# Kernel optimization log

Hardware: AMD Instinct MI355X
Metric: run time of the kernel (lower is better)

Reference implementation:

```python
import jax, jax.numpy as jnp
import numpy as np

INNER = 64  # hardcoded inner_dim in the torch module


def _knn_idx(pos, k):
    # dgcnn-style knn: topk of negative squared distance (includes self)
    d2 = jnp.sum(pos * pos, axis=-1)                      # (b, n)
    sim = 2.0 * jnp.einsum('bic,bjc->bij', pos, pos) - d2[:, :, None] - d2[:, None, :]
    return jax.lax.top_k(sim, k)[1]                       # (b, n, k)


def setup_inputs() -> dict:
    key = jax.random.key(0)
    ks = jax.random.split(key, 16)
    emb_dim = 256
    b, n, k = 8, 2048, 16
    s = 0.05
    inp = {
        'x': jax.random.normal(ks[0], (b, n, emb_dim), dtype=jnp.float32),
        'pos': jax.random.normal(ks[1], (b, n, 3), dtype=jnp.float32),
        'w_qkv': jax.random.normal(ks[2], (emb_dim, 3 * INNER), dtype=jnp.float32) * s,
        'w_pos1': jax.random.normal(ks[3], (3, 64), dtype=jnp.float32) * s,
        'b_pos1': jnp.zeros((64,), dtype=jnp.float32),
        'w_pos2': jax.random.normal(ks[4], (64, INNER), dtype=jnp.float32) * s,
        'b_pos2': jnp.zeros((INNER,), dtype=jnp.float32),
        'w_att1': jax.random.normal(ks[5], (INNER, 4 * INNER), dtype=jnp.float32) * s,
        'b_att1': jnp.zeros((4 * INNER,), dtype=jnp.float32),
        'w_att2': jax.random.normal(ks[6], (4 * INNER, INNER), dtype=jnp.float32) * s,
        'b_att2': jnp.zeros((INNER,), dtype=jnp.float32),
        'w_out': jax.random.normal(ks[7], (INNER, emb_dim), dtype=jnp.float32) * s,
        'b_out': jnp.zeros((emb_dim,), dtype=jnp.float32),
        'k': k,
    }
    return inp


def reference(x, pos, w_qkv, w_pos1, b_pos1, w_pos2, b_pos2,
              w_att1, b_att1, w_att2, b_att2, w_out, b_out, k):
    b, n, _ = x.shape
    qkv = x @ w_qkv                                        # (b, n, 3*INNER)
    q, kk, v = jnp.split(qkv, 3, axis=-1)                  # each (b, n, INNER)

    idx = _knn_idx(pos, k) + (jnp.arange(b) * n)[:, None, None]  # flat offsets
    idxf = idx.reshape(-1)

    def gather(t, d):
        return jnp.take(t.reshape(b * n, d), idxf, axis=0).reshape(b, n, k, d)

    pos_nn = gather(pos, 3)                                # (b, n, k, 3)
    rel_pos = pos_nn - pos[:, :, None, :]
    rpe = jax.nn.relu(rel_pos @ w_pos1 + b_pos1) @ w_pos2 + b_pos2  # (b, n, k, INNER)

    q_nn = gather(q, INNER)
    k_nn = gather(kk, INNER)
    v_nn = gather(v, INNER) + rpe

    h = q_nn - k_nn + rpe
    sim = jax.nn.relu(h @ w_att1 + b_att1) @ w_att2 + b_att2       # (b, n, k, INNER)

    # NOTE: faithful to torch source — softmax over the CHANNEL dim (-1),
    # then L2-normalize over the neighbor dim (-2).
    attn = jax.nn.softmax(sim, axis=-1)
    norm = jnp.sqrt(jnp.sum(attn * attn, axis=-2, keepdims=True))
    attn = attn / jnp.maximum(norm, 1e-12)

    agg = jnp.sum(attn * v_nn, axis=2)                     # (b, n, INNER)
    return agg @ w_out + b_out                             # (b, n, emb_dim)
```

## Files before the change

### kernel.cpp

```cpp
#include <hip/hip_runtime.h>
#include <stdint.h>

typedef __attribute__((ext_vector_type(8))) short bf8v;
typedef __attribute__((ext_vector_type(4))) float f4v;
typedef __attribute__((ext_vector_type(4))) unsigned int u4v;
typedef __attribute__((ext_vector_type(2))) unsigned int u2v;

#define MFMA16(a,b,c) __builtin_amdgcn_mfma_f32_16x16x32_bf16((a),(b),(c),0,0,0)

__device__ __forceinline__ unsigned short f2bf(float f) {
    unsigned u = __float_as_uint(f);
    return (unsigned short)((u + 0x7FFFu + ((u >> 16) & 1u)) >> 16);
}
#define SW(row,k,L) ((row)*(L) + ((k) ^ (((row)&7)<<3)))

#define WS_QMK   0u
#define WS_V     4194304u
#define WS_AGG   8388608u
#define WS_IDX   12582912u
#define WS_W1T   13631488u
#define WS_W2T   13664256u
#define WS_WPT   13697024u
#define WS_WQK   13705216u
#define WS_WOUT  13770752u

__global__ __launch_bounds__(256) void k_prep(
    const float* __restrict__ w_qkv, const float* __restrict__ w_pos2,
    const float* __restrict__ w_att1, const float* __restrict__ w_att2,
    const float* __restrict__ w_out, char* __restrict__ ws)
{
    int t = blockIdx.x * 256 + threadIdx.x;
    unsigned short* w1i = (unsigned short*)(ws + WS_W1T);
    unsigned short* w2i = (unsigned short*)(ws + WS_W2T);
    unsigned short* wpi = (unsigned short*)(ws + WS_WPT);
    unsigned short* wqi = (unsigned short*)(ws + WS_WQK);
    unsigned short* woi = (unsigned short*)(ws + WS_WOUT);
    if (t < 16384) {
        int hid = t >> 6, k = t & 63;
        w1i[hid*64 + (k ^ ((hid&7)<<3))] = f2bf(w_att1[k*256 + hid]);
    } else if (t < 32768) {
        int i = t - 16384; int ch = i >> 8, k = i & 255;
        w2i[ch*256 + (k ^ ((ch&7)<<3))] = f2bf(w_att2[k*64 + ch]);
    } else if (t < 36864) {
        int i = t - 32768; int ch = i >> 6, k = i & 63;
        wpi[ch*64 + (k ^ ((ch&7)<<3))] = f2bf(w_pos2[k*64 + ch]);
    } else if (t < 69632) {
        int i = t - 36864; int col = i >> 8, k = i & 255;
        float val = (col < 64) ? (w_qkv[k*192 + col] - w_qkv[k*192 + 64 + col])
                               : w_qkv[k*192 + 128 + (col - 64)];
        wqi[col*256 + (k ^ ((col&7)<<3))] = f2bf(val);
    } else if (t < 86016) {
        int i = t - 69632; int col = i >> 6, k = i & 63;
        woi[col*64 + (k ^ ((col&7)<<3))] = f2bf(w_out[k*256 + col]);
    }
}

__global__ __launch_bounds__(256) void k_knn(const float* __restrict__ pos,
                                             int* __restrict__ idxo) {
    const int wid = threadIdx.x >> 6, lane = threadIdx.x & 63;
    const int pid = blockIdx.x * 4 + wid;
    const int b = pid >> 11, i = pid & 2047;
    const float* pb = pos + (size_t)b * 2048 * 3;
    float xi = pb[i*3], yi = pb[i*3+1], zi = pb[i*3+2];
    float d2i = xi*xi; d2i = fmaf(yi, yi, d2i); d2i = fmaf(zi, zi, d2i);
    unsigned long long key[32];
#pragma unroll
    for (int m = 0; m < 32; ++m) {
        int j = m * 64 + lane;
        float xj = pb[j*3], yj = pb[j*3+1], zj = pb[j*3+2];
        float d2j = xj*xj; d2j = fmaf(yj, yj, d2j); d2j = fmaf(zj, zj, d2j);
        float dot = xi*xj; dot = fmaf(yi, yj, dot); dot = fmaf(zi, zj, dot);
        float sim = 2.0f*dot - d2i - d2j;
        unsigned u = __float_as_uint(sim);
        unsigned fk = (u & 0x80000000u) ? ~u : (u | 0x80000000u);
        key[m] = ((unsigned long long)fk << 32) | (unsigned)(0xFFFFFFFFu - (unsigned)j);
    }
    unsigned long long lmax = key[0];
#pragma unroll
    for (int m = 1; m < 32; ++m) lmax = (key[m] > lmax) ? key[m] : lmax;
    int my = 0;
    for (int it = 0; it < 16; ++it) {
        unsigned long long wmax = lmax;
#pragma unroll
        for (int st = 32; st >= 1; st >>= 1) {
            unsigned long long o = __shfl_xor(wmax, st);
            wmax = (o > wmax) ? o : wmax;
        }
        int jw = (int)(0xFFFFFFFFu - (unsigned)(wmax & 0xFFFFFFFFull));
        if (lane == it) my = jw;
        if (lmax == wmax) {
#pragma unroll
            for (int m = 0; m < 32; ++m) if (key[m] == wmax) key[m] = 0ull;
            lmax = key[0];
#pragma unroll
            for (int m = 1; m < 32; ++m) lmax = (key[m] > lmax) ? key[m] : lmax;
        }
    }
    if (lane < 16) idxo[pid * 16 + lane] = b * 2048 + my;
}

__global__ __launch_bounds__(256, 1) void k_qkv(const float* __restrict__ x,
        const char* __restrict__ wimg, float* __restrict__ qmk, float* __restrict__ v) {
    extern __shared__ char smem[];
    unsigned short* WQ = (unsigned short*)smem;
    unsigned short* XT = (unsigned short*)(smem + 65536);
    const int tid = threadIdx.x, wid = tid >> 6, lane = tid & 63;
    const int q4 = lane >> 4, l15 = lane & 15;
#pragma unroll
    for (int itn = 0; itn < 16; ++itn) {
        int off = itn * 4096 + tid * 16;
        *(u4v*)(smem + off) = *(const u4v*)(wimg + off);
    }
    __syncthreads();
    {
        int r = tid >> 2, k64 = (tid & 3) * 64;
        const float* xr = x + ((size_t)blockIdx.x * 64 + r) * 256 + k64;
#pragma unroll
        for (int c = 0; c < 8; ++c) {
            f4v a = *(const f4v*)(xr + c*8);
            f4v bq = *(const f4v*)(xr + c*8 + 4);
            bf8v s;
            s[0]=(short)f2bf(a[0]); s[1]=(short)f2bf(a[1]); s[2]=(short)f2bf(a[2]); s[3]=(short)f2bf(a[3]);
            s[4]=(short)f2bf(bq[0]); s[5]=(short)f2bf(bq[1]); s[6]=(short)f2bf(bq[2]); s[7]=(short)f2bf(bq[3]);
            *(bf8v*)&XT[SW(r, k64 + c*8, 256)] = s;
        }
    }
    f4v z = {0.f,0.f,0.f,0.f};
    f4v acc[8];
#pragma unroll
    for (int n = 0; n < 8; ++n) acc[n] = z;
    const int arow = wid*16 + l15;
#pragma unroll
    for (int ks = 0; ks < 8; ++ks) {
        int k0 = ks*32 + q4*8;
        bf8v a = *(const bf8v*)&XT[SW(arow, k0, 256)];
#pragma unroll
        for (int nt = 0; nt < 8; ++nt) {
            bf8v bq = *(const bf8v*)&WQ[SW(nt*16 + l15, k0, 256)];
            acc[nt] = MFMA16(a, bq, acc[nt]);
        }
    }
    size_t rbase = (size_t)blockIdx.x * 64 + wid*16 + q4*4;
#pragma unroll
    for (int nt = 0; nt < 8; ++nt) {
        int col = nt*16 + l15;
#pragma unroll
        for (int j = 0; j < 4; ++j) {
            if (nt < 4) qmk[(rbase + j)*64 + col] = acc[nt][j];
            else        v[(rbase + j)*64 + (col - 64)] = acc[nt][j];
        }
    }
}

__global__ __launch_bounds__(512, 2) void k_att(
    const float* __restrict__ qmk, const float* __restrict__ v,
    const float* __restrict__ pos, const int* __restrict__ idx,
    const float* __restrict__ w_pos1, const float* __restrict__ b_pos1,
    const float* __restrict__ b_pos2, const float* __restrict__ b_att1,
    const float* __restrict__ b_att2, const char* __restrict__ wblob,
    float* __restrict__ agg)
{
    extern __shared__ char smem[];
    unsigned short* W1T = (unsigned short*)smem;
    unsigned short* W2T = (unsigned short*)(smem + 32768);
    unsigned short* WPT = (unsigned short*)(smem + 65536);
    const int tid = threadIdx.x, wid = tid >> 6, lane = tid & 63;
    const int q4 = lane >> 4, l15 = lane & 15;
    const int r4 = lane >> 2, c16 = (lane & 3) * 16;
    char* wb = smem + 73728 + wid * 10240;
    unsigned short* P  = (unsigned short*)wb;
    unsigned short* PH = (unsigned short*)wb;
    unsigned short* H  = (unsigned short*)(wb + 8192);

#pragma unroll
    for (int it = 0; it < 9; ++it) {
        int off = it * 8192 + tid * 16;
        *(u4v*)(smem + off) = *(const u4v*)(wblob + off);
    }
    __syncthreads();

#pragma unroll 1
    for (int g = 0; g < 8; ++g) {
        const int p = (blockIdx.x * 8 + wid) * 8 + g;
        const int rowbase = p * 16;

        const int flat_l = idx[rowbase + l15];
        f4v qk[4], vv[4];
#pragma unroll
        for (int mt = 0; mt < 4; ++mt)
            qk[mt] = *(const f4v*)(qmk + (size_t)flat_l * 64 + mt*16 + q4*4);
#pragma unroll
        for (int mt = 0; mt < 4; ++mt)
            vv[mt] = *(const f4v*)(v + (size_t)flat_l * 64 + mt*16 + q4*4);

        {
            int flat_r = idx[rowbase + r4];
            float cx = pos[p*3], cy = pos[p*3+1], cz = pos[p*3+2];
            float r0 = pos[flat_r*3] - cx, r1 = pos[flat_r*3+1] - cy, r2v = pos[flat_r*3+2] - cz;
            bf8v lo, hi;
#pragma unroll
            for (int u = 0; u < 4; ++u) {
                f4v w0 = *(const f4v*)(w_pos1 + c16 + u*4);
                f4v w1 = *(const f4v*)(w_pos1 + 64 + c16 + u*4);
                f4v w2 = *(const f4v*)(w_pos1 + 128 + c16 + u*4);
                f4v bb = *(const f4v*)(b_pos1 + c16 + u*4);
#pragma unroll
                for (int j = 0; j < 4; ++j) {
                    float t = fmaf(r2v, w2[j], fmaf(r1, w1[j], fmaf(r0, w0[j], bb[j])));
                    t = fmaxf(t, 0.f);
                    if (u < 2) lo[u*4+j] = (short)f2bf(t);
                    else       hi[(u-2)*4+j] = (short)f2bf(t);
                }
            }
            *(bf8v*)&PH[SW(r4, c16, 64)] = lo;
            *(bf8v*)&PH[SW(r4, c16+8, 64)] = hi;
        }

        f4v rp[4];
#pragma unroll
        for (int mt = 0; mt < 4; ++mt) rp[mt] = *(const f4v*)(b_pos2 + mt*16 + q4*4);
#pragma unroll
        for (int ks = 0; ks < 2; ++ks) {
            int k0 = ks*32 + q4*8;
            bf8v bfr = *(const bf8v*)&PH[SW(l15, k0, 64)];
#pragma unroll
            for (int mt = 0; mt < 4; ++mt)
                rp[mt] = MFMA16(*(const bf8v*)&WPT[SW(mt*16+l15, k0, 64)], bfr, rp[mt]);
        }

        f4v vn[4];
#pragma unroll
        for (int mt = 0; mt < 4; ++mt) {
            float h0 = rp[mt][0] + qk[mt][0], h1 = rp[mt][1] + qk[mt][1];
            float h2 = rp[mt][2] + qk[mt][2], h3 = rp[mt][3] + qk[mt][3];
            u2v pp;
            pp[0] = (unsigned)f2bf(h0) | ((unsigned)f2bf(h1) << 16);
            pp[1] = (unsigned)f2bf(h2) | ((unsigned)f2bf(h3) << 16);
            *(u2v*)&H[SW(l15, mt*16 + q4*4, 64)] = pp;
            vn[mt] = rp[mt] + vv[mt];
        }

        f4v c1[16];
#pragma unroll
        for (int mt = 0; mt < 16; ++mt) c1[mt] = *(const f4v*)(b_att1 + mt*16 + q4*4);
#pragma unroll
        for (int ks = 0; ks < 2; ++ks) {
            int k0 = ks*32 + q4*8;
            bf8v bfr = *(const bf8v*)&H[SW(l15, k0, 64)];
#pragma unroll
            for (int mt = 0; mt < 16; ++mt)
                c1[mt] = MFMA16(*(const bf8v*)&W1T[SW(mt*16+l15, k0, 64)], bfr, c1[mt]);
        }

#pragma unroll
        for (int mt = 0; mt < 16; ++mt) {
            float t0 = fmaxf(c1[mt][0], 0.f), t1 = fmaxf(c1[mt][1], 0.f);
            float t2 = fmaxf(c1[mt][2], 0.f), t3 = fmaxf(c1[mt][3], 0.f);
            u2v pp;
            pp[0] = (unsigned)f2bf(t0) | ((unsigned)f2bf(t1) << 16);
            pp[1] = (unsigned)f2bf(t2) | ((unsigned)f2bf(t3) << 16);
            *(u2v*)&P[SW(l15, mt*16 + q4*4, 256)] = pp;
        }

        f4v ss[4];
#pragma unroll
        for (int mt = 0; mt < 4; ++mt) ss[mt] = *(const f4v*)(b_att2 + mt*16 + q4*4);
#pragma unroll
        for (int ks = 0; ks < 8; ++ks) {
            int k0 = ks*32 + q4*8;
            bf8v bfr = *(const bf8v*)&P[SW(l15, k0, 256)];
#pragma unroll
            for (int mt = 0; mt < 4; ++mt)
                ss[mt] = MFMA16(*(const bf8v*)&W2T[SW(mt*16+l15, k0, 256)], bfr, ss[mt]);
        }

        float e[16]; float mx = -3.4e38f;
#pragma unroll
        for (int i = 0; i < 16; ++i) { e[i] = ss[i>>2][i&3]; mx = fmaxf(mx, e[i]); }
        mx = fmaxf(mx, __shfl_xor(mx, 16));
        mx = fmaxf(mx, __shfl_xor(mx, 32));
        float sum = 0.f;
#pragma unroll
        for (int i = 0; i < 16; ++i) { e[i] = __expf(e[i] - mx); sum += e[i]; }
        sum += __shfl_xor(sum, 16);
        sum += __shfl_xor(sum, 32);
        float inv = 1.0f / sum;
        float nn[16], av[16];
#pragma unroll
        for (int i = 0; i < 16; ++i) {
            e[i] *= inv;
            nn[i] = e[i] * e[i];
            av[i] = e[i] * vn[i>>2][i&3];
        }
#pragma unroll
        for (int st = 1; st <= 8; st <<= 1) {
#pragma unroll
            for (int i = 0; i < 16; ++i) {
                nn[i] += __shfl_xor(nn[i], st);
                av[i] += __shfl_xor(av[i], st);
            }
        }
        if (l15 == 0) {
#pragma unroll
            for (int mt = 0; mt < 4; ++mt) {
                f4v o;
#pragma unroll
                for (int j = 0; j < 4; ++j)
                    o[j] = av[mt*4+j] / fmaxf(sqrtf(nn[mt*4+j]), 1e-12f);
                *(f4v*)(agg + (size_t)p*64 + mt*16 + q4*4) = o;
            }
        }
    }
}

__global__ __launch_bounds__(256, 1) void k_out(const float* __restrict__ agg,
        const char* __restrict__ wimg, const float* __restrict__ b_out,
        float* __restrict__ outp) {
    extern __shared__ char smem[];
    unsigned short* WO = (unsigned short*)smem;
    unsigned short* AT = (unsigned short*)(smem + 32768);
    const int tid = threadIdx.x, wid = tid >> 6, lane = tid & 63;
    const int q4 = lane >> 4, l15 = lane & 15;
#pragma unroll
    for (int itn = 0; itn < 8; ++itn) {
        int off = itn * 4096 + tid * 16;
        *(u4v*)(smem + off) = *(const u4v*)(wimg + off);
    }
    __syncthreads();
    {
        int r = tid >> 2, k16 = (tid & 3) * 16;
        const float* ar = agg + ((size_t)blockIdx.x * 64 + r) * 64 + k16;
        bf8v lo, hi;
#pragma unroll
        for (int i = 0; i < 16; ++i) {
            float t = ar[i];
            if (i < 8) lo[i] = (short)f2bf(t); else hi[i-8] = (short)f2bf(t);
        }
        *(bf8v*)&AT[SW(r, k16, 64)] = lo;
        *(bf8v*)&AT[SW(r, k16+8, 64)] = hi;
    }
    f4v z = {0.f,0.f,0.f,0.f};
    f4v acc[16];
#pragma unroll
    for (int nt = 0; nt < 16; ++nt) acc[nt] = z;
#pragma unroll
    for (int ks = 0; ks < 2; ++ks) {
        int k0 = ks*32 + q4*8;
        bf8v a = *(const bf8v*)&AT[SW(wid*16 + l15, k0, 64)];
#pragma unroll
        for (int nt = 0; nt < 16; ++nt) {
            bf8v bq = *(const bf8v*)&WO[SW(nt*16 + l15, k0, 64)];
            acc[nt] = MFMA16(a, bq, acc[nt]);
        }
    }
    size_t rbase = (size_t)blockIdx.x * 64 + wid*16 + q4*4;
#pragma unroll
    for (int nt = 0; nt < 16; ++nt) {
        int col = nt*16 + l15;
        float bo = b_out[col];
#pragma unroll
        for (int j = 0; j < 4; ++j)
            outp[(rbase + j)*256 + col] = acc[nt][j] + bo;
    }
}

extern "C" void kernel_launch(void* const* d_in, const int* in_sizes, int n_in,
                              void* d_out, int out_size, void* d_ws, size_t ws_size,
                              hipStream_t stream) {
    (void)in_sizes; (void)n_in; (void)out_size; (void)ws_size;
    const float* x      = (const float*)d_in[0];
    const float* pos    = (const float*)d_in[1];
    const float* w_qkv  = (const float*)d_in[2];
    const float* w_pos1 = (const float*)d_in[3];
    const float* b_pos1 = (const float*)d_in[4];
    const float* w_pos2 = (const float*)d_in[5];
    const float* b_pos2 = (const float*)d_in[6];
    const float* w_att1 = (const float*)d_in[7];
    const float* b_att1 = (const float*)d_in[8];
    const float* w_att2 = (const float*)d_in[9];
    const float* b_att2 = (const float*)d_in[10];
    const float* w_out  = (const float*)d_in[11];
    const float* b_out  = (const float*)d_in[12];
    float* outp = (float*)d_out;

    char* ws = (char*)d_ws;
    float* qmk = (float*)(ws + WS_QMK);
    float* v   = (float*)(ws + WS_V);
    float* agg = (float*)(ws + WS_AGG);
    int*   idx = (int*)(ws + WS_IDX);

    k_prep<<<dim3(336), dim3(256), 0, stream>>>(w_qkv, w_pos2, w_att1, w_att2, w_out, ws);
    k_knn<<<dim3(4096), dim3(256), 0, stream>>>(pos, idx);
    k_qkv<<<dim3(256), dim3(256), 98304, stream>>>(x, ws + WS_WQK, qmk, v);
    k_att<<<dim3(256), dim3(512), 155648, stream>>>(qmk, v, pos, idx,
                                                    w_pos1, b_pos1, b_pos2, b_att1, b_att2,
                                                    ws + WS_W1T, agg);
    k_out<<<dim3(256), dim3(256), 40960, stream>>>(agg, ws + WS_WOUT, b_out, outp);
}
```

Baseline: 581.6 us.

## Store q-k and v as bf16 with permuted layout to halve gather traffic

The QKV kernel now writes q-minus-k and v as bf16, staged through shared memory in a permuted column order so each attention lane reads its fragment with two 16-byte loads. The attention kernel gathers these bf16 rows instead of fp32, reuses the idx value through a shuffle, folds the v+rpe sum into the aggregation step, and splits the first MLP accumulator into two halves to lower register pressure. This targets gather bandwidth and register use in k_att. The cost is reduced precision on q-k and v and an extra shared-memory staging pass in k_qkv.

```diff
diff --git a/kernel.cpp b/kernel.cpp
--- a/kernel.cpp
+++ b/kernel.cpp
@@ -12,6 +12,8 @@
     unsigned u = __float_as_uint(f);
     return (unsigned short)((u + 0x7FFFu + ((u >> 16) & 1u)) >> 16);
 }
+__device__ __forceinline__ float bflo(unsigned w) { return __uint_as_float(w << 16); }
+__device__ __forceinline__ float bfhi(unsigned w) { return __uint_as_float(w & 0xFFFF0000u); }
 #define SW(row,k,L) ((row)*(L) + ((k) ^ (((row)&7)<<3)))
 
 #define WS_QMK   0u
@@ -100,10 +102,13 @@
 }
 
 __global__ __launch_bounds__(256, 1) void k_qkv(const float* __restrict__ x,
-        const char* __restrict__ wimg, float* __restrict__ qmk, float* __restrict__ v) {
+        const char* __restrict__ wimg, unsigned short* __restrict__ qb,
+        unsigned short* __restrict__ vb) {
     extern __shared__ char smem[];
     unsigned short* WQ = (unsigned short*)smem;
     unsigned short* XT = (unsigned short*)(smem + 65536);
+    unsigned short* BQ = (unsigned short*)(smem + 98304);
+    unsigned short* BV = (unsigned short*)(smem + 106496);
     const int tid = threadIdx.x, wid = tid >> 6, lane = tid & 63;
     const int q4 = lane >> 4, l15 = lane & 15;
 #pragma unroll
@@ -140,20 +145,30 @@
             acc[nt] = MFMA16(a, bq, acc[nt]);
         }
     }
-    size_t rbase = (size_t)blockIdx.x * 64 + wid*16 + q4*4;
 #pragma unroll
     for (int nt = 0; nt < 8; ++nt) {
-        int col = nt*16 + l15;
-#pragma unroll
-        for (int j = 0; j < 4; ++j) {
-            if (nt < 4) qmk[(rbase + j)*64 + col] = acc[nt][j];
-            else        v[(rbase + j)*64 + (col - 64)] = acc[nt][j];
-        }
+        int mt = nt & 3;
+        unsigned short* B = (nt < 4) ? BQ : BV;
+        int pp = (l15 >> 2) * 16 + mt * 4 + (l15 & 3);
+#pragma unroll
+        for (int j2 = 0; j2 < 4; ++j2) {
+            int rl = wid*16 + q4*4 + j2;
+            B[rl*64 + pp] = f2bf(acc[nt][j2]);
+        }
+    }
+    __syncthreads();
+    size_t base = (size_t)blockIdx.x * 64;
+#pragma unroll
+    for (int rep = 0; rep < 2; ++rep) {
+        int chunk = tid*2 + rep;
+        int row = chunk >> 3, c8 = chunk & 7;
+        *(u4v*)(qb + (base + row)*64 + c8*8) = *(const u4v*)&BQ[row*64 + c8*8];
+        *(u4v*)(vb + (base + row)*64 + c8*8) = *(const u4v*)&BV[row*64 + c8*8];
     }
 }
 
 __global__ __launch_bounds__(512, 2) void k_att(
-    const float* __restrict__ qmk, const float* __restrict__ v,
+    const unsigned short* __restrict__ qb, const unsigned short* __restrict__ vb,
     const float* __restrict__ pos, const int* __restrict__ idx,
     const float* __restrict__ w_pos1, const float* __restrict__ b_pos1,
     const float* __restrict__ b_pos2, const float* __restrict__ b_att1,
@@ -185,16 +200,11 @@
         const int rowbase = p * 16;
 
         const int flat_l = idx[rowbase + l15];
-        f4v qk[4], vv[4];
-#pragma unroll
-        for (int mt = 0; mt < 4; ++mt)
-            qk[mt] = *(const f4v*)(qmk + (size_t)flat_l * 64 + mt*16 + q4*4);
-#pragma unroll
-        for (int mt = 0; mt < 4; ++mt)
-            vv[mt] = *(const f4v*)(v + (size_t)flat_l * 64 + mt*16 + q4*4);
+        u4v qkp0 = *(const u4v*)(qb + (size_t)flat_l*64 + q4*16);
+        u4v qkp1 = *(const u4v*)(qb + (size_t)flat_l*64 + q4*16 + 8);
 
         {
-            int flat_r = idx[rowbase + r4];
+            int flat_r = __shfl(flat_l, r4);
             float cx = pos[p*3], cy = pos[p*3+1], cz = pos[p*3+2];
             float r0 = pos[flat_r*3] - cx, r1 = pos[flat_r*3+1] - cy, r2v = pos[flat_r*3+2] - cz;
             bf8v lo, hi;
@@ -228,38 +238,46 @@
                 rp[mt] = MFMA16(*(const bf8v*)&WPT[SW(mt*16+l15, k0, 64)], bfr, rp[mt]);
         }
 
-        f4v vn[4];
+#define QW(w) ((w) < 4 ? qkp0[(w)] : qkp1[(w)-4])
 #pragma unroll
         for (int mt = 0; mt < 4; ++mt) {
-            float h0 = rp[mt][0] + qk[mt][0], h1 = rp[mt][1] + qk[mt][1];
-            float h2 = rp[mt][2] + qk[mt][2], h3 = rp[mt][3] + qk[mt][3];
+            float h0 = rp[mt][0] + bflo(QW(mt*2));
+            float h1 = rp[mt][1] + bfhi(QW(mt*2));
+            float h2 = rp[mt][2] + bflo(QW(mt*2+1));
+            float h3 = rp[mt][3] + bfhi(QW(mt*2+1));
             u2v pp;
             pp[0] = (unsigned)f2bf(h0) | ((unsigned)f2bf(h1) << 16);
             pp[1] = (unsigned)f2bf(h2) | ((unsigned)f2bf(h3) << 16);
             *(u2v*)&H[SW(l15, mt*16 + q4*4, 64)] = pp;
-            vn[mt] = rp[mt] + vv[mt];
-        }
-
-        f4v c1[16];
-#pragma unroll
-        for (int mt = 0; mt < 16; ++mt) c1[mt] = *(const f4v*)(b_att1 + mt*16 + q4*4);
-#pragma unroll
-        for (int ks = 0; ks < 2; ++ks) {
-            int k0 = ks*32 + q4*8;
-            bf8v bfr = *(const bf8v*)&H[SW(l15, k0, 64)];
-#pragma unroll
-            for (int mt = 0; mt < 16; ++mt)
-                c1[mt] = MFMA16(*(const bf8v*)&W1T[SW(mt*16+l15, k0, 64)], bfr, c1[mt]);
-        }
-
-#pragma unroll
-        for (int mt = 0; mt < 16; ++mt) {
-            float t0 = fmaxf(c1[mt][0], 0.f), t1 = fmaxf(c1[mt][1], 0.f);
-            float t2 = fmaxf(c1[mt][2], 0.f), t3 = fmaxf(c1[mt][3], 0.f);
-            u2v pp;
-            pp[0] = (unsigned)f2bf(t0) | ((unsigned)f2bf(t1) << 16);
-            pp[1] = (unsigned)f2bf(t2) | ((unsigned)f2bf(t3) << 16);
-            *(u2v*)&P[SW(l15, mt*16 + q4*4, 256)] = pp;
+        }
+#undef QW
+        u4v vvp0 = *(const u4v*)(vb + (size_t)flat_l*64 + q4*16);
+        u4v vvp1 = *(const u4v*)(vb + (size_t)flat_l*64 + q4*16 + 8);
+
+#pragma unroll
+        for (int hf = 0; hf < 2; ++hf) {
+            f4v c1h[8];
+#pragma unroll
+            for (int m = 0; m < 8; ++m)
+                c1h[m] = *(const f4v*)(b_att1 + (hf*8 + m)*16 + q4*4);
+#pragma unroll
+            for (int ks = 0; ks < 2; ++ks) {
+                int k0 = ks*32 + q4*8;
+                bf8v bfr = *(const bf8v*)&H[SW(l15, k0, 64)];
+#pragma unroll
+                for (int m = 0; m < 8; ++m)
+                    c1h[m] = MFMA16(*(const bf8v*)&W1T[SW((hf*8+m)*16+l15, k0, 64)], bfr, c1h[m]);
+            }
+#pragma unroll
+            for (int m = 0; m < 8; ++m) {
+                int mtg = hf*8 + m;
+                float t0 = fmaxf(c1h[m][0], 0.f), t1 = fmaxf(c1h[m][1], 0.f);
+                float t2 = fmaxf(c1h[m][2], 0.f), t3 = fmaxf(c1h[m][3], 0.f);
+                u2v pp;
+                pp[0] = (unsigned)f2bf(t0) | ((unsigned)f2bf(t1) << 16);
+                pp[1] = (unsigned)f2bf(t2) | ((unsigned)f2bf(t3) << 16);
+                *(u2v*)&P[SW(l15, mtg*16 + q4*4, 256)] = pp;
+            }
         }
 
         f4v ss[4];
@@ -286,12 +304,16 @@
         sum += __shfl_xor(sum, 32);
         float inv = 1.0f / sum;
         float nn[16], av[16];
+#define VW(w) ((w) < 4 ? vvp0[(w)] : vvp1[(w)-4])
 #pragma unroll
         for (int i = 0; i < 16; ++i) {
+            int mt = i >> 2, j = i & 3;
+            float vf = (j & 1) ? bfhi(VW(mt*2 + (j>>1))) : bflo(VW(mt*2 + (j>>1)));
             e[i] *= inv;
             nn[i] = e[i] * e[i];
-            av[i] = e[i] * vn[i>>2][i&3];
-        }
+            av[i] = e[i] * (rp[mt][j] + vf);
+        }
+#undef VW
 #pragma unroll
         for (int st = 1; st <= 8; st <<= 1) {
 #pragma unroll
@@ -384,15 +406,15 @@
     float* outp = (float*)d_out;
 
     char* ws = (char*)d_ws;
-    float* qmk = (float*)(ws + WS_QMK);
-    float* v   = (float*)(ws + WS_V);
+    unsigned short* qb = (unsigned short*)(ws + WS_QMK);
+    unsigned short* vb = (unsigned short*)(ws + WS_V);
     float* agg = (float*)(ws + WS_AGG);
     int*   idx = (int*)(ws + WS_IDX);
 
     k_prep<<<dim3(336), dim3(256), 0, stream>>>(w_qkv, w_pos2, w_att1, w_att2, w_out, ws);
     k_knn<<<dim3(4096), dim3(256), 0, stream>>>(pos, idx);
-    k_qkv<<<dim3(256), dim3(256), 98304, stream>>>(x, ws + WS_WQK, qmk, v);
-    k_att<<<dim3(256), dim3(512), 155648, stream>>>(qmk, v, pos, idx,
+    k_qkv<<<dim3(256), dim3(256), 114688, stream>>>(x, ws + WS_WQK, qb, vb);
+    k_att<<<dim3(256), dim3(512), 155648, stream>>>(qb, vb, pos, idx,
                                                     w_pos1, b_pos1, b_pos2, b_att1, b_att2,
                                                     ws + WS_W1T, agg);
     k_out<<<dim3(256), dim3(256), 40960, stream>>>(agg, ws + WS_WOUT, b_out, outp);
```

Result: slower. 651.3 us (+12.0%).
